# Optimization experiments

Measured on AMD Instinct MI355X. Metric: run time of the kernel, lower is better.

The kernel has to match this reference:

```python
import jax, jax.numpy as jnp
import numpy as np

B = 8
D = 512        # d_hidn
H = 8          # n_head
DH = 64        # d_head
L = 6          # n_layer
DFF = 2048     # d_ff
GRID = 10
DMLP = 1024
NOUT = 1
EPS = 1e-6
CIN = 2048
SEQ = 1 + 24 * 32 + 9 * 12 + 5 * 7  # 912


def setup_inputs() -> dict:
    key = jax.random.key(0)
    ks = jax.random.split(key, 40)
    rn = lambda k, s, sc=0.02: jax.random.normal(k, s, jnp.float32) * sc
    inp = {
        "feat_dis_org": jax.random.normal(ks[0], (B, CIN, 24, 32), jnp.float32),
        "feat_dis_ref_1": jax.random.normal(ks[1], (B, CIN, 9, 12), jnp.float32),
        "feat_dis_ref_2": jax.random.normal(ks[2], (B, CIN, 5, 7), jnp.float32),
        "conv_w": rn(ks[3], (D, CIN)),
        "conv_b": rn(ks[4], (D,)),
        "scale_org_emb": jax.random.uniform(ks[5], (D,), jnp.float32),
        "ref_1_emb": jax.random.uniform(ks[6], (D,), jnp.float32),
        "ref_2_emb": rn(ks[7], (D,), 1.0),
        "pos_emb": rn(ks[8], (GRID, GRID, D), 0.02),
        "cls_token": rn(ks[9], (D,), 0.02),
        "Wq": rn(ks[10], (L, D, D)), "bq": rn(ks[11], (L, D)),
        "Wk": rn(ks[12], (L, D, D)), "bk": rn(ks[13], (L, D)),
        "Wv": rn(ks[14], (L, D, D)), "bv": rn(ks[15], (L, D)),
        "Wo": rn(ks[16], (L, D, D)), "bo": rn(ks[17], (L, D)),
        "ln1_g": jnp.ones((L, D), jnp.float32), "ln1_b": jnp.zeros((L, D), jnp.float32),
        "w1": rn(ks[18], (L, DFF, D)), "b1": rn(ks[19], (L, DFF)),
        "w2": rn(ks[20], (L, D, DFF)), "b2": rn(ks[21], (L, D)),
        "ln2_g": jnp.ones((L, D), jnp.float32), "ln2_b": jnp.zeros((L, D), jnp.float32),
        "proj_w1": rn(ks[22], (DMLP, D)),
        "proj_w2": rn(ks[23], (NOUT, DMLP)),
        "mask_inputs": jnp.ones((B, SEQ), jnp.int32),
    }
    return inp


def _ln(x, g, b):
    m = jnp.mean(x, -1, keepdims=True)
    v = jnp.mean((x - m) ** 2, -1, keepdims=True)
    return (x - m) * jax.lax.rsqrt(v + EPS) * g + b


def _embed(feat, chan_emb, conv_w, conv_b, pos_emb):
    # 1x1 conv (conv_enc) as a channel contraction: [b,2048,h,w] -> [b,D,h,w]
    x = jnp.einsum('bchw,dc->bdhw', feat, conv_w) + conv_b[None, :, None, None]
    x = x + chan_emb[None, :, None, None]           # scale/ref embedding
    h, w = x.shape[2], x.shape[3]
    # vectorized version of the nested-loop gather: t_i = int(i/h*Grid)
    ti = (jnp.arange(h) * GRID) // h
    tj = (jnp.arange(w) * GRID) // w
    sp = pos_emb[ti][:, tj]                          # [h,w,D]
    x = x + jnp.transpose(sp, (2, 0, 1))[None]       # [b,D,h,w]
    return jnp.transpose(x.reshape(x.shape[0], D, h * w), (0, 2, 1))  # [b,hw,D]


def reference(feat_dis_org, feat_dis_ref_1, feat_dis_ref_2, conv_w, conv_b,
              scale_org_emb, ref_1_emb, ref_2_emb, pos_emb, cls_token,
              Wq, bq, Wk, bk, Wv, bv, Wo, bo, ln1_g, ln1_b,
              w1, b1, w2, b2, ln2_g, ln2_b, proj_w1, proj_w2, mask_inputs):
    t_org = _embed(feat_dis_org, scale_org_emb, conv_w, conv_b, pos_emb)
    t_r1 = _embed(feat_dis_ref_1, ref_1_emb, conv_w, conv_b, pos_emb)
    t_r2 = _embed(feat_dis_ref_2, ref_2_emb, conv_w, conv_b, pos_emb)
    cls = jnp.broadcast_to(cls_token[None, None, :], (B, 1, D))
    x = jnp.concatenate([cls, t_org, t_r1, t_r2], axis=1)   # [B,SEQ,D]

    pad = (mask_inputs == 0)[:, None, None, :]              # [B,1,1,SEQ]
    scale = 1.0 / (DH ** 0.5)

    for i in range(L):
        s = x.shape[1]
        q = (x @ Wq[i].T + bq[i]).reshape(B, s, H, DH).transpose(0, 2, 1, 3)
        k = (x @ Wk[i].T + bk[i]).reshape(B, s, H, DH).transpose(0, 2, 1, 3)
        v = (x @ Wv[i].T + bv[i]).reshape(B, s, H, DH).transpose(0, 2, 1, 3)
        scores = jnp.einsum('bhqd,bhkd->bhqk', q, k) * scale
        scores = jnp.where(pad, -1e9, scores)
        prob = jax.nn.softmax(scores, axis=-1)
        ctx = jnp.einsum('bhqk,bhkd->bhqd', prob, v)
        ctx = ctx.transpose(0, 2, 1, 3).reshape(B, s, H * DH)
        att = ctx @ Wo[i].T + bo[i]
        x = _ln(x + att, ln1_g[i], ln1_b[i])
        ff = jax.nn.gelu(x @ w1[i].T + b1[i], approximate=False) @ w2[i].T + b2[i]
        x = _ln(x + ff, ln2_g[i], ln2_b[i])

    cls_out = x[:, 0, :]
    hmlp = jax.nn.gelu(cls_out @ proj_w1.T, approximate=False)
    pred = hmlp @ proj_w2.T                                   # [B,1]
    return pred
```

## Files before the change

kernel.cpp:

```cpp
#include <hip/hip_runtime.h>
#include <hip/hip_bf16.h>
#include <math.h>

#define SEQ 912
#define NTOK 911
#define CIN_ 2048
#define NLAYER 6

typedef _Float16 f16x8 __attribute__((ext_vector_type(8)));
typedef _Float16 f16x4 __attribute__((ext_vector_type(4)));
typedef float f32x4 __attribute__((ext_vector_type(4)));

__device__ __forceinline__ float gelu_f(float x) {
    return 0.5f * x * (1.0f + erff(x * 0.70710678118654752f));
}

template <int ACT, int QKV>
__global__ __launch_bounds__(256) void gemm16(
    const _Float16* __restrict__ A, const _Float16* __restrict__ B,
    const float* __restrict__ bias, _Float16* __restrict__ Cout,
    _Float16* __restrict__ vT, int M, int N, int K, int ldc)
{
    constexpr int BK = 32;
    __shared__ __align__(16) char smem[20480];
    _Float16* As = (_Float16*)smem;
    _Float16* Bs = As + 128 * 40;
    _Float16* Cs = (_Float16*)smem;
    const int t = threadIdx.x;
    const int m0 = blockIdx.y * 128, n0 = blockIdx.x * 128;
    const int lane = t & 63, w = t >> 6;
    const int r0 = (w >> 1) * 64, c0 = (w & 1) * 64;
    const int ln15 = lane & 15, quad = lane >> 4;
    const int srow = t >> 2, schunk = (t & 3) * 8;

    f32x4 zero = {0.f, 0.f, 0.f, 0.f};
    f32x4 acc[4][4];
#pragma unroll
    for (int i = 0; i < 4; ++i)
#pragma unroll
        for (int j = 0; j < 4; ++j) acc[i][j] = zero;

    float4 pa[2], pb[2];
#pragma unroll
    for (int p = 0; p < 2; ++p) {
        int m = p * 64 + srow;
        int gm = m0 + m, gn = n0 + m;
        pa[p] = make_float4(0.f, 0.f, 0.f, 0.f);
        pb[p] = make_float4(0.f, 0.f, 0.f, 0.f);
        if (gm < M) pa[p] = *(const float4*)(A + (size_t)gm * K + schunk);
        if (gn < N) pb[p] = *(const float4*)(B + (size_t)gn * K + schunk);
    }

    for (int k0 = 0; k0 < K; k0 += BK) {
#pragma unroll
        for (int p = 0; p < 2; ++p) {
            int m = p * 64 + srow;
            *(float4*)&As[m * 40 + schunk] = pa[p];
            *(float4*)&Bs[m * 40 + schunk] = pb[p];
        }
        __syncthreads();
        int k1 = k0 + BK;
        if (k1 < K) {
#pragma unroll
            for (int p = 0; p < 2; ++p) {
                int m = p * 64 + srow;
                int gm = m0 + m, gn = n0 + m;
                pa[p] = make_float4(0.f, 0.f, 0.f, 0.f);
                pb[p] = make_float4(0.f, 0.f, 0.f, 0.f);
                if (gm < M) pa[p] = *(const float4*)(A + (size_t)gm * K + k1 + schunk);
                if (gn < N) pb[p] = *(const float4*)(B + (size_t)gn * K + k1 + schunk);
            }
        }
        f16x8 a[4], b[4];
#pragma unroll
        for (int i = 0; i < 4; ++i)
            a[i] = *(const f16x8*)&As[(r0 + i * 16 + ln15) * 40 + quad * 8];
#pragma unroll
        for (int j = 0; j < 4; ++j)
            b[j] = *(const f16x8*)&Bs[(c0 + j * 16 + ln15) * 40 + quad * 8];
#pragma unroll
        for (int i = 0; i < 4; ++i)
#pragma unroll
            for (int j = 0; j < 4; ++j)
                acc[i][j] = __builtin_amdgcn_mfma_f32_16x16x32_f16(a[i], b[j], acc[i][j], 0, 0, 0);
        __syncthreads();
    }

    if (QKV && n0 >= 1024) {
#pragma unroll
        for (int j = 0; j < 4; ++j) {
            int gn = n0 + c0 + j * 16 + ln15;
            float bv = bias[gn];
            int chan = gn - 1024;
            int hh = chan >> 6, d = chan & 63;
#pragma unroll
            for (int i = 0; i < 4; ++i) {
                int gmBase = m0 + r0 + i * 16 + quad * 4;
                int bb = gmBase / 912, s = gmBase - bb * 912;
                f16x4 hv4;
#pragma unroll
                for (int r = 0; r < 4; ++r) hv4[r] = (_Float16)(acc[i][j][r] + bv);
                *(f16x4*)&vT[((size_t)((bb * 8 + hh) * 64 + d)) * 960 + s] = hv4;
            }
        }
    } else {
#pragma unroll
        for (int half = 0; half < 2; ++half) {
            if ((w >> 1) == half) {
#pragma unroll
                for (int j = 0; j < 4; ++j) {
                    float bv = bias[n0 + c0 + j * 16 + ln15];
#pragma unroll
                    for (int i = 0; i < 4; ++i)
#pragma unroll
                        for (int r = 0; r < 4; ++r) {
                            float val = acc[i][j][r] + bv;
                            if (ACT == 1) val = gelu_f(val);
                            Cs[(i * 16 + quad * 4 + r) * 136 + c0 + j * 16 + ln15] = (_Float16)val;
                        }
                }
            }
            __syncthreads();
#pragma unroll
            for (int uu = 0; uu < 4; ++uu) {
                int u = t + uu * 256;
                int lr = u >> 4, ch = (u & 15) * 8;
                int gm = m0 + half * 64 + lr;
                if (gm < M)
                    *(f16x8*)&Cout[(size_t)gm * ldc + n0 + ch] = *(const f16x8*)&Cs[lr * 136 + ch];
            }
            __syncthreads();
        }
    }
}

__global__ __launch_bounds__(256) void gemm16_splitk(
    const _Float16* __restrict__ A, const _Float16* __restrict__ B,
    float* __restrict__ part, int M, int N, int K)
{
    constexpr int BK = 32;
    __shared__ __align__(16) _Float16 As[128 * 40];
    __shared__ __align__(16) _Float16 Bs[64 * 40];
    const int t = threadIdx.x;
    const int m0 = blockIdx.y * 128, n0 = blockIdx.x * 64;
    const int z = blockIdx.z;
    const int lane = t & 63, w = t >> 6;
    const int r0 = (w >> 1) * 64, c0 = (w & 1) * 32;
    const int ln15 = lane & 15, quad = lane >> 4;
    const int srow = t >> 2, schunk = (t & 3) * 8;
    const int Ks = K >> 1;
    const int kBeg = z * Ks, kEnd = kBeg + Ks;

    f32x4 zero = {0.f, 0.f, 0.f, 0.f};
    f32x4 acc[4][2];
#pragma unroll
    for (int i = 0; i < 4; ++i)
#pragma unroll
        for (int j = 0; j < 2; ++j) acc[i][j] = zero;

    float4 pa[2], pb;
#pragma unroll
    for (int p = 0; p < 2; ++p) {
        int m = p * 64 + srow;
        int gm = m0 + m;
        pa[p] = make_float4(0.f, 0.f, 0.f, 0.f);
        if (gm < M) pa[p] = *(const float4*)(A + (size_t)gm * K + kBeg + schunk);
    }
    {
        int gn = n0 + srow;
        pb = make_float4(0.f, 0.f, 0.f, 0.f);
        if (gn < N) pb = *(const float4*)(B + (size_t)gn * K + kBeg + schunk);
    }

    for (int k0 = kBeg; k0 < kEnd; k0 += BK) {
#pragma unroll
        for (int p = 0; p < 2; ++p) {
            int m = p * 64 + srow;
            *(float4*)&As[m * 40 + schunk] = pa[p];
        }
        *(float4*)&Bs[srow * 40 + schunk] = pb;
        __syncthreads();
        int k1 = k0 + BK;
        if (k1 < kEnd) {
#pragma unroll
            for (int p = 0; p < 2; ++p) {
                int m = p * 64 + srow;
                int gm = m0 + m;
                pa[p] = make_float4(0.f, 0.f, 0.f, 0.f);
                if (gm < M) pa[p] = *(const float4*)(A + (size_t)gm * K + k1 + schunk);
            }
            int gn = n0 + srow;
            pb = make_float4(0.f, 0.f, 0.f, 0.f);
            if (gn < N) pb = *(const float4*)(B + (size_t)gn * K + k1 + schunk);
        }
        f16x8 a[4], b[2];
#pragma unroll
        for (int i = 0; i < 4; ++i)
            a[i] = *(const f16x8*)&As[(r0 + i * 16 + ln15) * 40 + quad * 8];
#pragma unroll
        for (int j = 0; j < 2; ++j)
            b[j] = *(const f16x8*)&Bs[(c0 + j * 16 + ln15) * 40 + quad * 8];
#pragma unroll
        for (int i = 0; i < 4; ++i)
#pragma unroll
            for (int j = 0; j < 2; ++j)
                acc[i][j] = __builtin_amdgcn_mfma_f32_16x16x32_f16(a[i], b[j], acc[i][j], 0, 0, 0);
        __syncthreads();
    }

    float* out = part + (size_t)z * M * N;
#pragma unroll
    for (int j = 0; j < 2; ++j) {
        int gn = n0 + c0 + j * 16 + ln15;
#pragma unroll
        for (int i = 0; i < 4; ++i) {
            int gmBase = m0 + r0 + i * 16 + quad * 4;
#pragma unroll
            for (int r = 0; r < 4; ++r) {
                int gm = gmBase + r;
                if (gm < M) out[(size_t)gm * N + gn] = acc[i][j][r];
            }
        }
    }
}

__global__ __launch_bounds__(256) void cast16_kernel(
    const float* __restrict__ src, _Float16* __restrict__ dst, int n4)
{
    int i = blockIdx.x * 256 + threadIdx.x;
    if (i < n4) {
        float4 v = ((const float4*)src)[i];
        f16x4 h;
        h[0] = (_Float16)v.x; h[1] = (_Float16)v.y;
        h[2] = (_Float16)v.z; h[3] = (_Float16)v.w;
        ((f16x4*)dst)[i] = h;
    }
}

__global__ __launch_bounds__(256) void cast2_kernel(
    const float* __restrict__ s1, _Float16* __restrict__ d1, int n4_1,
    const float* __restrict__ s2, _Float16* __restrict__ d2, int n4_2)
{
    int i = blockIdx.x * 256 + threadIdx.x;
    if (i < n4_1) {
        float4 v = ((const float4*)s1)[i];
        f16x4 h;
        h[0] = (_Float16)v.x; h[1] = (_Float16)v.y;
        h[2] = (_Float16)v.z; h[3] = (_Float16)v.w;
        ((f16x4*)d1)[i] = h;
    } else {
        int j = i - n4_1;
        if (j < n4_2) {
            float4 v = ((const float4*)s2)[j];
            f16x4 h;
            h[0] = (_Float16)v.x; h[1] = (_Float16)v.y;
            h[2] = (_Float16)v.z; h[3] = (_Float16)v.w;
            ((f16x4*)d2)[j] = h;
        }
    }
}

__global__ __launch_bounds__(256) void pack_qkvw_kernel(
    const float* __restrict__ Wq, const float* __restrict__ Wk,
    const float* __restrict__ Wv, _Float16* __restrict__ dst)
{
    int idx = blockIdx.x * 256 + threadIdx.x;
    if (idx >= 6 * 1536 * 128) return;
    int c4 = idx & 127;
    int rc = idx >> 7;
    int r = rc % 1536;
    int l = rc / 1536;
    const float* src = (r < 512) ? Wq : (r < 1024) ? Wk : Wv;
    float4 v = *(const float4*)(src + ((size_t)l * 512 + (r & 511)) * 512 + c4 * 4);
    f16x4 h;
    h[0] = (_Float16)v.x; h[1] = (_Float16)v.y;
    h[2] = (_Float16)v.z; h[3] = (_Float16)v.w;
    *(f16x4*)(dst + ((size_t)l * 1536 + r) * 512 + c4 * 4) = h;
}

__global__ __launch_bounds__(256) void pack_qkvb_kernel(
    const float* __restrict__ bq, const float* __restrict__ bk,
    const float* __restrict__ bv, float* __restrict__ dst)
{
    int idx = blockIdx.x * 256 + threadIdx.x;
    if (idx < 6 * 1536) {
        int r = idx % 1536, l = idx / 1536;
        const float* s = (r < 512) ? bq : (r < 1024) ? bk : bv;
        dst[idx] = s[l * 512 + (r & 511)];
    }
}

__global__ __launch_bounds__(256) void transpose_feat_kernel(
    const float* __restrict__ feat, _Float16* __restrict__ patch, int HW, int tok_off)
{
    __shared__ float tile[32][33];
    const int b = blockIdx.z;
    const int c0 = blockIdx.y * 32;
    const int p0 = blockIdx.x * 32;
    const int tx = threadIdx.x, ty = threadIdx.y;
#pragma unroll
    for (int i = 0; i < 4; ++i) {
        int c = c0 + ty + i * 8;
        int p = p0 + tx;
        tile[ty + i * 8][tx] = (p < HW) ? feat[((size_t)b * CIN_ + c) * HW + p] : 0.f;
    }
    __syncthreads();
#pragma unroll
    for (int i = 0; i < 4; ++i) {
        int p = p0 + ty + i * 8;
        int c = c0 + tx;
        if (p < HW)
            patch[((size_t)(b * NTOK + tok_off + p)) * CIN_ + c] = (_Float16)tile[tx][ty + i * 8];
    }
}

__global__ __launch_bounds__(128) void build_x_red(
    const float* __restrict__ part, const float* __restrict__ conv_b,
    const float* __restrict__ cls_token,
    const float* __restrict__ emb_org, const float* __restrict__ emb_r1,
    const float* __restrict__ emb_r2, const float* __restrict__ pos_emb,
    float* __restrict__ x, _Float16* __restrict__ x16)
{
    const size_t ESTR = (size_t)7288 * 512;
    const int row = blockIdx.x;
    const int b = row / SEQ;
    const int tt = row - b * SEQ;
    const int d4 = threadIdx.x;
    float4 o;
    if (tt == 0) {
        o = ((const float4*)cls_token)[d4];
    } else {
        int tp = tt - 1;
        const float* ce; int hh, ww, p;
        if (tp < 768)      { p = tp;       hh = 24; ww = 32; ce = emb_org; }
        else if (tp < 876) { p = tp - 768; hh = 9;  ww = 12; ce = emb_r1; }
        else               { p = tp - 876; hh = 5;  ww = 7;  ce = emb_r2; }
        int i = p / ww, j = p - i * ww;
        int ti = (i * 10) / hh, tj = (j * 10) / ww;
        size_t prow = (size_t)(b * NTOK + tp) * 512;
        float4 t0 = ((const float4*)(part + prow))[d4];
        float4 t1 = ((const float4*)(part + ESTR + prow))[d4];
        float4 cb = ((const float4*)conv_b)[d4];
        float4 cv = ((const float4*)ce)[d4];
        float4 pv = ((const float4*)(pos_emb + (size_t)(ti * 10 + tj) * 512))[d4];
        o.x = t0.x + t1.x + cb.x + cv.x + pv.x;
        o.y = t0.y + t1.y + cb.y + cv.y + pv.y;
        o.z = t0.z + t1.z + cb.z + cv.z + pv.z;
        o.w = t0.w + t1.w + cb.w + cv.w + pv.w;
    }
    ((float4*)(x + (size_t)row * 512))[d4] = o;
    f16x4 h;
    h[0] = (_Float16)o.x; h[1] = (_Float16)o.y;
    h[2] = (_Float16)o.z; h[3] = (_Float16)o.w;
    ((f16x4*)(x16 + (size_t)row * 512))[d4] = h;
}

__global__ __launch_bounds__(64) void ln_residual_red(
    float* __restrict__ x, _Float16* __restrict__ x16,
    const float* __restrict__ part, const float* __restrict__ bias,
    const float* __restrict__ g, const float* __restrict__ bta)
{
    const size_t LSTR = (size_t)7296 * 512;
    const int row = blockIdx.x;
    const int t = threadIdx.x;
    float4* xr = (float4*)(x + (size_t)row * 512);
    const float4* p0 = (const float4*)(part + (size_t)row * 512);
    const float4* p1 = (const float4*)(part + LSTR + (size_t)row * 512);
    const float4* bb = (const float4*)bias;
    float4 a0 = xr[t], a1 = xr[t + 64];
    float4 q0 = p0[t], q1 = p0[t + 64];
    float4 r0 = p1[t], r1 = p1[t + 64];
    float4 c0 = bb[t], c1 = bb[t + 64];
    a0.x += q0.x + r0.x + c0.x; a0.y += q0.y + r0.y + c0.y;
    a0.z += q0.z + r0.z + c0.z; a0.w += q0.w + r0.w + c0.w;
    a1.x += q1.x + r1.x + c1.x; a1.y += q1.y + r1.y + c1.y;
    a1.z += q1.z + r1.z + c1.z; a1.w += q1.w + r1.w + c1.w;
    float s = a0.x + a0.y + a0.z + a0.w + a1.x + a1.y + a1.z + a1.w;
#pragma unroll
    for (int o = 32; o; o >>= 1) s += __shfl_xor(s, o, 64);
    const float mean = s * (1.f / 512.f);
    float sq = 0.f;
    sq += (a0.x - mean) * (a0.x - mean); sq += (a0.y - mean) * (a0.y - mean);
    sq += (a0.z - mean) * (a0.z - mean); sq += (a0.w - mean) * (a0.w - mean);
    sq += (a1.x - mean) * (a1.x - mean); sq += (a1.y - mean) * (a1.y - mean);
    sq += (a1.z - mean) * (a1.z - mean); sq += (a1.w - mean) * (a1.w - mean);
#pragma unroll
    for (int o = 32; o; o >>= 1) sq += __shfl_xor(sq, o, 64);
    const float rstd = rsqrtf(sq * (1.f / 512.f) + 1e-6f);
    const float4 g0 = ((const float4*)g)[t], g1 = ((const float4*)g)[t + 64];
    const float4 e0 = ((const float4*)bta)[t], e1 = ((const float4*)bta)[t + 64];
    float4 o0, o1;
    o0.x = (a0.x - mean) * rstd * g0.x + e0.x;
    o0.y = (a0.y - mean) * rstd * g0.y + e0.y;
    o0.z = (a0.z - mean) * rstd * g0.z + e0.z;
    o0.w = (a0.w - mean) * rstd * g0.w + e0.w;
    o1.x = (a1.x - mean) * rstd * g1.x + e1.x;
    o1.y = (a1.y - mean) * rstd * g1.y + e1.y;
    o1.z = (a1.z - mean) * rstd * g1.z + e1.z;
    o1.w = (a1.w - mean) * rstd * g1.w + e1.w;
    xr[t] = o0; xr[t + 64] = o1;
    f16x4 h0, h1;
    h0[0] = (_Float16)o0.x; h0[1] = (_Float16)o0.y;
    h0[2] = (_Float16)o0.z; h0[3] = (_Float16)o0.w;
    h1[0] = (_Float16)o1.x; h1[1] = (_Float16)o1.y;
    h1[2] = (_Float16)o1.z; h1[3] = (_Float16)o1.w;
    f16x4* xh = (f16x4*)(x16 + (size_t)row * 512);
    xh[t] = h0; xh[t + 64] = h1;
}

__global__ __launch_bounds__(256) void attn_mfma(
    const _Float16* __restrict__ qk, const _Float16* __restrict__ vT,
    const int* __restrict__ mask, _Float16* __restrict__ ctx)
{
    __shared__ __align__(16) _Float16 Ks[64 * 72];
    __shared__ __align__(16) _Float16 VTs[64 * 72];
    __shared__ __align__(16) _Float16 Pw[4][16 * 72];
    __shared__ float biasS[64];
    const int qt = blockIdx.x, h = blockIdx.y, b = blockIdx.z;
    const int q0 = qt * 64;
    const int t = threadIdx.x;
    const int wave = t >> 6, lane = t & 63;
    const int ln15 = lane & 15, quad = lane >> 4;
    const int qrow = q0 + wave * 16 + ln15;

    f16x8 qf[2];
#pragma unroll
    for (int ks = 0; ks < 2; ++ks) {
        f16x8 z = {0, 0, 0, 0, 0, 0, 0, 0};
        qf[ks] = (qrow < SEQ)
            ? *(const f16x8*)(qk + (size_t)(b * SEQ + qrow) * 1024 + h * 64 + ks * 32 + quad * 8)
            : z;
    }

    f32x4 oacc[4];
    f32x4 zero = {0.f, 0.f, 0.f, 0.f};
#pragma unroll
    for (int dj = 0; dj < 4; ++dj) oacc[dj] = zero;
    float m_i = -1e30f, l_i = 0.f;

    for (int kb = 0; kb < 960; kb += 64) {
#pragma unroll
        for (int i = 0; i < 2; ++i) {
            int u = t + i * 256;
            int r = u >> 3, ch = (u & 7) * 8;
            int kg = kb + r;
            f16x8 kvv = {0, 0, 0, 0, 0, 0, 0, 0};
            if (kg < SEQ) kvv = *(const f16x8*)(qk + (size_t)(b * SEQ + kg) * 1024 + 512 + h * 64 + ch);
            *(f16x8*)&Ks[r * 72 + ch] = kvv;
            f16x8 vv = {0, 0, 0, 0, 0, 0, 0, 0};
            if (kb + ch < SEQ)
                vv = *(const f16x8*)(vT + ((size_t)((b * 8 + h) * 64 + r)) * 960 + kb + ch);
            *(f16x8*)&VTs[r * 72 + ch] = vv;
        }
        if (t < 64) {
            int kg = kb + t;
            biasS[t] = (kg < SEQ) ? (mask[b * SEQ + kg] ? 0.f : -1e9f) : -2e9f;
        }
        __syncthreads();

        f32x4 st[4];
#pragma unroll
        for (int jj = 0; jj < 4; ++jj) st[jj] = zero;
#pragma unroll
        for (int jj = 0; jj < 4; ++jj)
#pragma unroll
            for (int ks = 0; ks < 2; ++ks) {
                f16x8 kf = *(const f16x8*)&Ks[(jj * 16 + ln15) * 72 + ks * 32 + quad * 8];
                st[jj] = __builtin_amdgcn_mfma_f32_16x16x32_f16(kf, qf[ks], st[jj], 0, 0, 0);
            }

        float p[4][4];
        float mloc = -3e38f;
#pragma unroll
        for (int jj = 0; jj < 4; ++jj) {
            f32x4 bfr = *(const f32x4*)&biasS[jj * 16 + quad * 4];
#pragma unroll
            for (int r = 0; r < 4; ++r) {
                float sv = st[jj][r] * 0.125f + bfr[r];
                p[jj][r] = sv;
                mloc = fmaxf(mloc, sv);
            }
        }
        mloc = fmaxf(mloc, __shfl_xor(mloc, 16, 64));
        mloc = fmaxf(mloc, __shfl_xor(mloc, 32, 64));
        float mnew = fmaxf(m_i, mloc);
        float alpha = __expf(m_i - mnew);
        m_i = mnew;
        float sloc = 0.f;
#pragma unroll
        for (int jj = 0; jj < 4; ++jj)
#pragma unroll
            for (int r = 0; r < 4; ++r) {
                p[jj][r] = __expf(p[jj][r] - mnew);
                sloc += p[jj][r];
            }
        sloc += __shfl_xor(sloc, 16, 64);
        sloc += __shfl_xor(sloc, 32, 64);
        l_i = l_i * alpha + sloc;

        float ar[4];
#pragma unroll
        for (int r = 0; r < 4; ++r) ar[r] = __shfl(alpha, quad * 4 + r, 64);
#pragma unroll
        for (int dj = 0; dj < 4; ++dj)
#pragma unroll
            for (int r = 0; r < 4; ++r) oacc[dj][r] *= ar[r];

        _Float16* pw = &Pw[wave][0];
#pragma unroll
        for (int jj = 0; jj < 4; ++jj)
#pragma unroll
            for (int r = 0; r < 4; ++r)
                pw[ln15 * 72 + jj * 16 + quad * 4 + r] = (_Float16)p[jj][r];
        f16x8 pf[2];
#pragma unroll
        for (int ks = 0; ks < 2; ++ks)
            pf[ks] = *(const f16x8*)&pw[ln15 * 72 + ks * 32 + quad * 8];

#pragma unroll
        for (int dj = 0; dj < 4; ++dj)
#pragma unroll
            for (int ks = 0; ks < 2; ++ks) {
                f16x8 vf = *(const f16x8*)&VTs[(dj * 16 + ln15) * 72 + ks * 32 + quad * 8];
                oacc[dj] = __builtin_amdgcn_mfma_f32_16x16x32_f16(pf[ks], vf, oacc[dj], 0, 0, 0);
            }
        __syncthreads();
    }

    float linv[4];
#pragma unroll
    for (int r = 0; r < 4; ++r) linv[r] = 1.f / __shfl(l_i, quad * 4 + r, 64);
#pragma unroll
    for (int dj = 0; dj < 4; ++dj)
#pragma unroll
        for (int r = 0; r < 4; ++r) {
            int row = q0 + wave * 16 + quad * 4 + r;
            if (row < SEQ)
                ctx[(size_t)(b * SEQ + row) * 512 + h * 64 + dj * 16 + ln15] =
                    (_Float16)(oacc[dj][r] * linv[r]);
        }
}

__global__ __launch_bounds__(64) void head1_kernel(
    const float* __restrict__ x, const float* __restrict__ w,
    float* __restrict__ hmlp)
{
    const int n = blockIdx.x & 1023;
    const int b = blockIdx.x >> 10;
    const int t = threadIdx.x;
    const float4* cls = (const float4*)(x + (size_t)b * SEQ * 512);
    const float4* wr = (const float4*)(w + (size_t)n * 512);
    float s = 0.f;
#pragma unroll
    for (int i = 0; i < 2; ++i) {
        float4 a = cls[t + i * 64], c = wr[t + i * 64];
        s += a.x * c.x + a.y * c.y + a.z * c.z + a.w * c.w;
    }
#pragma unroll
    for (int o = 32; o; o >>= 1) s += __shfl_xor(s, o, 64);
    if (t == 0) hmlp[b * 1024 + n] = gelu_f(s);
}

__global__ __launch_bounds__(256) void head2_kernel(
    const float* __restrict__ hmlp, const float* __restrict__ w,
    float* __restrict__ out)
{
    __shared__ float red[4];
    const int b = blockIdx.x;
    const int t = threadIdx.x;
    float s = 0.f;
    for (int i = t; i < 1024; i += 256) s += hmlp[b * 1024 + i] * w[i];
#pragma unroll
    for (int o = 32; o; o >>= 1) s += __shfl_xor(s, o, 64);
    if ((t & 63) == 0) red[t >> 6] = s;
    __syncthreads();
    if (t == 0) out[b] = red[0] + red[1] + red[2] + red[3];
}

extern "C" void kernel_launch(void* const* d_in, const int* in_sizes, int n_in,
                              void* d_out, int out_size, void* d_ws, size_t ws_size,
                              hipStream_t stream)
{
    const float* feat_org = (const float*)d_in[0];
    const float* feat_r1  = (const float*)d_in[1];
    const float* feat_r2  = (const float*)d_in[2];
    const float* conv_w   = (const float*)d_in[3];
    const float* conv_b   = (const float*)d_in[4];
    const float* emb_org  = (const float*)d_in[5];
    const float* emb_r1   = (const float*)d_in[6];
    const float* emb_r2   = (const float*)d_in[7];
    const float* pos_emb  = (const float*)d_in[8];
    const float* cls_tok  = (const float*)d_in[9];
    const float* Wq = (const float*)d_in[10];
    const float* bq = (const float*)d_in[11];
    const float* Wk = (const float*)d_in[12];
    const float* bk = (const float*)d_in[13];
    const float* Wv = (const float*)d_in[14];
    const float* bv = (const float*)d_in[15];
    const float* Wo = (const float*)d_in[16];
    const float* bo = (const float*)d_in[17];
    const float* ln1g = (const float*)d_in[18];
    const float* ln1b = (const float*)d_in[19];
    const float* w1 = (const float*)d_in[20];
    const float* b1 = (const float*)d_in[21];
    const float* w2 = (const float*)d_in[22];
    const float* b2 = (const float*)d_in[23];
    const float* ln2g = (const float*)d_in[24];
    const float* ln2b = (const float*)d_in[25];
    const float* pw1 = (const float*)d_in[26];
    const float* pw2 = (const float*)d_in[27];
    const int*   mask = (const int*)d_in[28];

    char* base = (char*)d_ws;
    _Float16* ffh16 = (_Float16*)base;
    _Float16* patch16 = ffh16;
    base += (size_t)7296 * 2048 * 2;
    float* x = (float*)base; base += (size_t)7296 * 512 * 4;
    _Float16* qk16 = (_Float16*)base; base += (size_t)7296 * 1024 * 2;
    _Float16* vT16 = (_Float16*)base; base += (size_t)8 * 8 * 64 * 960 * 2;
    _Float16* ctx16 = (_Float16*)base; base += (size_t)7296 * 512 * 2;
    _Float16* x16   = (_Float16*)base; base += (size_t)7296 * 512 * 2;
    _Float16* wqkv_all = (_Float16*)base; base += (size_t)6 * 1536 * 512 * 2;
    _Float16* wo_all   = (_Float16*)base; base += (size_t)6 * 512 * 512 * 2;
    _Float16* w1_l16   = (_Float16*)base; base += (size_t)2048 * 512 * 2;
    _Float16* w2_l16   = (_Float16*)base; base += (size_t)512 * 2048 * 2;
    float* bqkv_all = (float*)base; base += 6 * 1536 * 4;
    float* hmlp = (float*)base; base += 8 * 1024 * 4;

    float* partO = (float*)ffh16;
    float* partF = (float*)qk16;
    _Float16* convw16 = x16;

    dim3 tb(32, 8);
    hipLaunchKernelGGL(transpose_feat_kernel, dim3(24, 64, 8), tb, 0, stream,
                       feat_org, patch16, 768, 0);
    hipLaunchKernelGGL(transpose_feat_kernel, dim3(4, 64, 8), tb, 0, stream,
                       feat_r1, patch16, 108, 768);
    hipLaunchKernelGGL(transpose_feat_kernel, dim3(2, 64, 8), tb, 0, stream,
                       feat_r2, patch16, 35, 876);
    hipLaunchKernelGGL(cast16_kernel, dim3(1024), 256, 0, stream,
                       conv_w, convw16, 512 * 2048 / 4);
    hipLaunchKernelGGL(cast16_kernel, dim3(1536), 256, 0, stream,
                       Wo, wo_all, 6 * 512 * 512 / 4);
    hipLaunchKernelGGL(pack_qkvw_kernel, dim3(4608), 256, 0, stream,
                       Wq, Wk, Wv, wqkv_all);
    hipLaunchKernelGGL(pack_qkvb_kernel, dim3(36), 256, 0, stream,
                       bq, bk, bv, bqkv_all);

    hipLaunchKernelGGL(gemm16_splitk, dim3(8, 57, 2), 256, 0, stream,
                       patch16, convw16, partF, 7288, 512, 2048);
    hipLaunchKernelGGL(build_x_red, dim3(7296), 128, 0, stream,
                       partF, conv_b, cls_tok, emb_org, emb_r1, emb_r2, pos_emb, x, x16);

    for (int l = 0; l < NLAYER; ++l) {
        hipLaunchKernelGGL(cast2_kernel, dim3(2048), 256, 0, stream,
                           w1 + (size_t)l * 2048 * 512, w1_l16, 2048 * 512 / 4,
                           w2 + (size_t)l * 512 * 2048, w2_l16, 512 * 2048 / 4);
        hipLaunchKernelGGL((gemm16<0, 1>), dim3(12, 57), 256, 0, stream,
                           x16, wqkv_all + (size_t)l * 1536 * 512, bqkv_all + l * 1536,
                           qk16, vT16, 7296, 1536, 512, 1024);
        hipLaunchKernelGGL(attn_mfma, dim3(15, 8, 8), 256, 0, stream,
                           qk16, vT16, mask, ctx16);
        hipLaunchKernelGGL(gemm16_splitk, dim3(8, 57, 2), 256, 0, stream,
                           ctx16, wo_all + (size_t)l * 512 * 512, partO, 7296, 512, 512);
        hipLaunchKernelGGL(ln_residual_red, dim3(7296), 64, 0, stream,
                           x, x16, partO, bo + l * 512, ln1g + l * 512, ln1b + l * 512);
        hipLaunchKernelGGL((gemm16<1, 0>), dim3(16, 57), 256, 0, stream,
                           x16, w1_l16, b1 + l * 2048,
                           ffh16, (_Float16*)nullptr, 7296, 2048, 512, 2048);
        hipLaunchKernelGGL(gemm16_splitk, dim3(8, 57, 2), 256, 0, stream,
                           ffh16, w2_l16, partF, 7296, 512, 2048);
        hipLaunchKernelGGL(ln_residual_red, dim3(7296), 64, 0, stream,
                           x, x16, partF, b2 + l * 512, ln2g + l * 512, ln2b + l * 512);
    }

    hipLaunchKernelGGL(head1_kernel, dim3(8 * 1024), 64, 0, stream, x, pw1, hmlp);
    hipLaunchKernelGGL(head2_kernel, dim3(8), 256, 0, stream, hmlp, pw2, (float*)d_out);
}
```

Baseline: 1.536 ms.

## Stage GEMM tiles with direct global-to-LDS loads and double buffering

```diff
diff --git a/kernel.cpp b/kernel.cpp
--- a/kernel.cpp
+++ b/kernel.cpp
@@ -13,6 +13,37 @@
 
 __device__ __forceinline__ float gelu_f(float x) {
     return 0.5f * x * (1.0f + erff(x * 0.70710678118654752f));
+}
+
+__device__ __forceinline__ void gld16(const _Float16* g, _Float16* l) {
+    __builtin_amdgcn_global_load_lds(
+        (const __attribute__((address_space(1))) unsigned int*)g,
+        (__attribute__((address_space(3))) unsigned int*)l,
+        16, 0, 0);
+}
+
+__device__ __forceinline__ void stage_tile_g(const _Float16* Ab, const _Float16* Bb,
+                                             size_t seg, _Float16* ldsW, int kk) {
+    gld16(Ab + kk, ldsW);
+    gld16(Ab + seg + kk, ldsW + 2048);
+    gld16(Bb + kk, ldsW + 4096);
+    gld16(Bb + seg + kk, ldsW + 6144);
+}
+
+__device__ __forceinline__ void compute_step_g(const _Float16* sb, int r0, int c0,
+                                               int ln15, int quad, f32x4 (&acc)[4][4]) {
+    f16x8 a[4], b[4];
+#pragma unroll
+    for (int i = 0; i < 4; ++i)
+        a[i] = *(const f16x8*)&sb[(r0 + i * 16 + ln15) * 32 + quad * 8];
+#pragma unroll
+    for (int j = 0; j < 4; ++j)
+        b[j] = *(const f16x8*)&sb[4096 + (c0 + j * 16 + ln15) * 32 + quad * 8];
+#pragma unroll
+    for (int i = 0; i < 4; ++i)
+#pragma unroll
+        for (int j = 0; j < 4; ++j)
+            acc[i][j] = __builtin_amdgcn_mfma_f32_16x16x32_f16(a[i], b[j], acc[i][j], 0, 0, 0);
 }
 
 template <int ACT, int QKV>
@@ -21,17 +52,13 @@
     const float* __restrict__ bias, _Float16* __restrict__ Cout,
     _Float16* __restrict__ vT, int M, int N, int K, int ldc)
 {
-    constexpr int BK = 32;
-    __shared__ __align__(16) char smem[20480];
-    _Float16* As = (_Float16*)smem;
-    _Float16* Bs = As + 128 * 40;
-    _Float16* Cs = (_Float16*)smem;
+    __shared__ __align__(16) _Float16 smem[2 * 8192];
+    _Float16* Cs = smem;
     const int t = threadIdx.x;
     const int m0 = blockIdx.y * 128, n0 = blockIdx.x * 128;
     const int lane = t & 63, w = t >> 6;
     const int r0 = (w >> 1) * 64, c0 = (w & 1) * 64;
     const int ln15 = lane & 15, quad = lane >> 4;
-    const int srow = t >> 2, schunk = (t & 3) * 8;
 
     f32x4 zero = {0.f, 0.f, 0.f, 0.f};
     f32x4 acc[4][4];
@@ -40,49 +67,21 @@
 #pragma unroll
         for (int j = 0; j < 4; ++j) acc[i][j] = zero;
 
-    float4 pa[2], pb[2];
-#pragma unroll
-    for (int p = 0; p < 2; ++p) {
-        int m = p * 64 + srow;
-        int gm = m0 + m, gn = n0 + m;
-        pa[p] = make_float4(0.f, 0.f, 0.f, 0.f);
-        pb[p] = make_float4(0.f, 0.f, 0.f, 0.f);
-        if (gm < M) pa[p] = *(const float4*)(A + (size_t)gm * K + schunk);
-        if (gn < N) pb[p] = *(const float4*)(B + (size_t)gn * K + schunk);
-    }
-
-    for (int k0 = 0; k0 < K; k0 += BK) {
-#pragma unroll
-        for (int p = 0; p < 2; ++p) {
-            int m = p * 64 + srow;
-            *(float4*)&As[m * 40 + schunk] = pa[p];
-            *(float4*)&Bs[m * 40 + schunk] = pb[p];
-        }
+    const _Float16* Ab = A + (size_t)(m0 + w * 16 + (lane >> 2)) * K + (lane & 3) * 8;
+    const _Float16* Bb = B + (size_t)(n0 + w * 16 + (lane >> 2)) * K + (lane & 3) * 8;
+    const size_t seg = (size_t)64 * K;
+    _Float16* ldsW = smem + w * 512;
+
+    stage_tile_g(Ab, Bb, seg, ldsW, 0);
+    __syncthreads();
+
+    const int nK = K >> 5;
+    for (int s = 0; s < nK; s += 2) {
+        stage_tile_g(Ab, Bb, seg, ldsW + 8192, (s + 1) << 5);
+        compute_step_g(smem, r0, c0, ln15, quad, acc);
         __syncthreads();
-        int k1 = k0 + BK;
-        if (k1 < K) {
-#pragma unroll
-            for (int p = 0; p < 2; ++p) {
-                int m = p * 64 + srow;
-                int gm = m0 + m, gn = n0 + m;
-                pa[p] = make_float4(0.f, 0.f, 0.f, 0.f);
-                pb[p] = make_float4(0.f, 0.f, 0.f, 0.f);
-                if (gm < M) pa[p] = *(const float4*)(A + (size_t)gm * K + k1 + schunk);
-                if (gn < N) pb[p] = *(const float4*)(B + (size_t)gn * K + k1 + schunk);
-            }
-        }
-        f16x8 a[4], b[4];
-#pragma unroll
-        for (int i = 0; i < 4; ++i)
-            a[i] = *(const f16x8*)&As[(r0 + i * 16 + ln15) * 40 + quad * 8];
-#pragma unroll
-        for (int j = 0; j < 4; ++j)
-            b[j] = *(const f16x8*)&Bs[(c0 + j * 16 + ln15) * 40 + quad * 8];
-#pragma unroll
-        for (int i = 0; i < 4; ++i)
-#pragma unroll
-            for (int j = 0; j < 4; ++j)
-                acc[i][j] = __builtin_amdgcn_mfma_f32_16x16x32_f16(a[i], b[j], acc[i][j], 0, 0, 0);
+        if (s + 2 < nK) stage_tile_g(Ab, Bb, seg, ldsW, (s + 2) << 5);
+        compute_step_g(smem + 8192, r0, c0, ln15, quad, acc);
         __syncthreads();
     }
 
@@ -134,22 +133,42 @@
     }
 }
 
+__device__ __forceinline__ void stage_tile_s(const _Float16* Ab, const _Float16* Bb,
+                                             size_t seg, _Float16* ldsW, int kk) {
+    gld16(Ab + kk, ldsW);
+    gld16(Ab + seg + kk, ldsW + 2048);
+    gld16(Bb + kk, ldsW + 4096);
+}
+
+__device__ __forceinline__ void compute_step_s(const _Float16* sb, int r0, int c0,
+                                               int ln15, int quad, f32x4 (&acc)[4][2]) {
+    f16x8 a[4], b[2];
+#pragma unroll
+    for (int i = 0; i < 4; ++i)
+        a[i] = *(const f16x8*)&sb[(r0 + i * 16 + ln15) * 32 + quad * 8];
+#pragma unroll
+    for (int j = 0; j < 2; ++j)
+        b[j] = *(const f16x8*)&sb[4096 + (c0 + j * 16 + ln15) * 32 + quad * 8];
+#pragma unroll
+    for (int i = 0; i < 4; ++i)
+#pragma unroll
+        for (int j = 0; j < 2; ++j)
+            acc[i][j] = __builtin_amdgcn_mfma_f32_16x16x32_f16(a[i], b[j], acc[i][j], 0, 0, 0);
+}
+
 __global__ __launch_bounds__(256) void gemm16_splitk(
     const _Float16* __restrict__ A, const _Float16* __restrict__ B,
     float* __restrict__ part, int M, int N, int K)
 {
-    constexpr int BK = 32;
-    __shared__ __align__(16) _Float16 As[128 * 40];
-    __shared__ __align__(16) _Float16 Bs[64 * 40];
+    __shared__ __align__(16) _Float16 smem[2 * 6144];
     const int t = threadIdx.x;
     const int m0 = blockIdx.y * 128, n0 = blockIdx.x * 64;
     const int z = blockIdx.z;
     const int lane = t & 63, w = t >> 6;
     const int r0 = (w >> 1) * 64, c0 = (w & 1) * 32;
     const int ln15 = lane & 15, quad = lane >> 4;
-    const int srow = t >> 2, schunk = (t & 3) * 8;
     const int Ks = K >> 1;
-    const int kBeg = z * Ks, kEnd = kBeg + Ks;
+    const int kBeg = z * Ks;
 
     f32x4 zero = {0.f, 0.f, 0.f, 0.f};
     f32x4 acc[4][2];
@@ -158,53 +177,21 @@
 #pragma unroll
         for (int j = 0; j < 2; ++j) acc[i][j] = zero;
 
-    float4 pa[2], pb;
-#pragma unroll
-    for (int p = 0; p < 2; ++p) {
-        int m = p * 64 + srow;
-        int gm = m0 + m;
-        pa[p] = make_float4(0.f, 0.f, 0.f, 0.f);
-        if (gm < M) pa[p] = *(const float4*)(A + (size_t)gm * K + kBeg + schunk);
-    }
-    {
-        int gn = n0 + srow;
-        pb = make_float4(0.f, 0.f, 0.f, 0.f);
-        if (gn < N) pb = *(const float4*)(B + (size_t)gn * K + kBeg + schunk);
-    }
-
-    for (int k0 = kBeg; k0 < kEnd; k0 += BK) {
-#pragma unroll
-        for (int p = 0; p < 2; ++p) {
-            int m = p * 64 + srow;
-            *(float4*)&As[m * 40 + schunk] = pa[p];
-        }
-        *(float4*)&Bs[srow * 40 + schunk] = pb;
+    const _Float16* Ab = A + (size_t)(m0 + w * 16 + (lane >> 2)) * K + kBeg + (lane & 3) * 8;
+    const _Float16* Bb = B + (size_t)(n0 + w * 16 + (lane >> 2)) * K + kBeg + (lane & 3) * 8;
+    const size_t seg = (size_t)64 * K;
+    _Float16* ldsW = smem + w * 512;
+
+    stage_tile_s(Ab, Bb, seg, ldsW, 0);
+    __syncthreads();
+
+    const int nK = Ks >> 5;
+    for (int s = 0; s < nK; s += 2) {
+        stage_tile_s(Ab, Bb, seg, ldsW + 6144, (s + 1) << 5);
+        compute_step_s(smem, r0, c0, ln15, quad, acc);
         __syncthreads();
-        int k1 = k0 + BK;
-        if (k1 < kEnd) {
-#pragma unroll
-            for (int p = 0; p < 2; ++p) {
-                int m = p * 64 + srow;
-                int gm = m0 + m;
-                pa[p] = make_float4(0.f, 0.f, 0.f, 0.f);
-                if (gm < M) pa[p] = *(const float4*)(A + (size_t)gm * K + k1 + schunk);
-            }
-            int gn = n0 + srow;
-            pb = make_float4(0.f, 0.f, 0.f, 0.f);
-            if (gn < N) pb = *(const float4*)(B + (size_t)gn * K + k1 + schunk);
-        }
-        f16x8 a[4], b[2];
-#pragma unroll
-        for (int i = 0; i < 4; ++i)
-            a[i] = *(const f16x8*)&As[(r0 + i * 16 + ln15) * 40 + quad * 8];
-#pragma unroll
-        for (int j = 0; j < 2; ++j)
-            b[j] = *(const f16x8*)&Bs[(c0 + j * 16 + ln15) * 40 + quad * 8];
-#pragma unroll
-        for (int i = 0; i < 4; ++i)
-#pragma unroll
-            for (int j = 0; j < 2; ++j)
-                acc[i][j] = __builtin_amdgcn_mfma_f32_16x16x32_f16(a[i], b[j], acc[i][j], 0, 0, 0);
+        if (s + 2 < nK) stage_tile_s(Ab, Bb, seg, ldsW, (s + 2) << 5);
+        compute_step_s(smem + 6144, r0, c0, ln15, quad, acc);
         __syncthreads();
     }
 
```

Result: no change. 1.506 ms (-1.9%).
